# Kernel tuning notes

Hardware: AMD Instinct MI355X
Metric: run time of the kernel (lower is better)

The kernel has to match this reference:

```python
import jax, jax.numpy as jnp
import numpy as np

N = 50000          # site nodes
L = 32             # max URL token length
E = 64             # embed_size
H = 128            # hidden_size
E_SIM = 800000     # edges per relation in blocks
E_SUB = 200000     # 'sim' edges classified at the end
NEG = 0.01         # LeakyReLU negative slope

def leaky(x):
    return jnp.where(x >= 0, x, NEG * x)

def lstm_final(x, mask, Wih, Whh, b, reverse):
    # x: [N, L, E], mask: [N, L] bool. Returns packed-sequence final hidden [N, E].
    if reverse:
        x = x[:, ::-1, :]
        mask = mask[:, ::-1]
    h0 = jnp.zeros((x.shape[0], Whh.shape[1]), x.dtype)
    def step(carry, inp):
        h, c = carry
        xt, mt = inp
        g = xt @ Wih.T + h @ Whh.T + b
        i, f, gg, o = jnp.split(g, 4, axis=-1)  # PyTorch gate order i,f,g,o
        cn = jax.nn.sigmoid(f) * c + jax.nn.sigmoid(i) * jnp.tanh(gg)
        hn = jax.nn.sigmoid(o) * jnp.tanh(cn)
        m = mt[:, None]
        return (jnp.where(m, hn, h), jnp.where(m, cn, c)), None
    (h, _), _ = jax.lax.scan(step, (h0, h0), (x.transpose(1, 0, 2), mask.T))
    return h

def graph_conv(h, src, dst, W, b):
    # DGL GraphConv, norm='both': D_dst^{-1/2} A D_src^{-1/2} h W + b  (degrees clamped to >=1)
    n = h.shape[0]
    ones = jnp.ones(src.shape[0], h.dtype)
    out_deg = jnp.clip(jax.ops.segment_sum(ones, src, num_segments=n), 1.0)
    in_deg = jnp.clip(jax.ops.segment_sum(ones, dst, num_segments=n), 1.0)
    feat = h * jax.lax.rsqrt(out_deg)[:, None]
    if W.shape[0] > W.shape[1]:
        feat = feat @ W  # project before gather/scatter when in_dim > out_dim (as DGL does)
        rst = jax.ops.segment_sum(feat[src], dst, num_segments=n)
    else:
        rst = jax.ops.segment_sum(feat[src], dst, num_segments=n) @ W
    return rst * jax.lax.rsqrt(in_deg)[:, None] + b

def setup_inputs():
    key = jax.random.key(0)
    ks = iter(jax.random.split(key, 64))
    def nrm(shape, scale=0.05):
        return jax.random.normal(next(ks), shape, dtype=jnp.float32) * scale
    inp = {}
    inp["inputs_s"] = jax.random.randint(next(ks), (N, L), 0, 128)
    lengths = jax.random.randint(next(ks), (N,), 1, L + 1)
    inp["inputs_sm"] = (jnp.arange(L)[None, :] < lengths[:, None]).astype(jnp.int32)
    inp["inputs_c"] = jax.random.randint(next(ks), (N, 1), 0, 101)
    inp["inputs_co"] = jax.random.randint(next(ks), (N, 1), 0, 92)
    inp["inputs_sl"] = jax.random.randint(next(ks), (N, 1), 0, 6)
    for name, m in [("sim_src", E_SIM), ("sim_dst", E_SIM), ("user_src", E_SIM),
                    ("user_dst", E_SIM), ("esub_src", E_SUB), ("esub_dst", E_SUB)]:
        inp[name] = jax.random.randint(next(ks), (m,), 0, N)
    inp["emb_url"] = nrm((128, E)); inp["emb_cat"] = nrm((101, E))
    inp["emb_country"] = nrm((92, E)); inp["emb_sl"] = nrm((6, E))
    for d in ("f", "b"):
        inp["Wih_" + d] = nrm((4 * E, E)); inp["Whh_" + d] = nrm((4 * E, E))
        inp["b_" + d] = nrm((4 * E,))  # b_ih + b_hh folded into one bias
    inp["fc_W"] = nrm((E, 2 * E)); inp["fc_b"] = nrm((E,))
    for i, din in enumerate([4 * E, H]):
        for rel in ("sim", "user"):
            inp["gcn%d_%s_W" % (i, rel)] = nrm((din, H))
            inp["gcn%d_%s_b" % (i, rel)] = nrm((H,))
    inp["cls_W1"] = nrm((H, 2 * H)); inp["cls_b1"] = nrm((H,))
    inp["bn_g"] = jnp.ones((H,), jnp.float32); inp["bn_b"] = jnp.zeros((H,), jnp.float32)
    inp["cls_W2"] = nrm((2, H)); inp["cls_b2"] = nrm((2,))
    return inp

def reference(inputs_s, inputs_sm, inputs_c, inputs_co, inputs_sl,
              sim_src, sim_dst, user_src, user_dst, esub_src, esub_dst,
              emb_url, emb_cat, emb_country, emb_sl,
              Wih_f, Whh_f, b_f, Wih_b, Whh_b, b_b, fc_W, fc_b,
              gcn0_sim_W, gcn0_sim_b, gcn0_user_W, gcn0_user_b,
              gcn1_sim_W, gcn1_sim_b, gcn1_user_W, gcn1_user_b,
              cls_W1, cls_b1, bn_g, bn_b, cls_W2, cls_b2):
    mask = inputs_sm.astype(bool)
    x = emb_url[inputs_s]                                # [N, L, E]
    hf = lstm_final(x, mask, Wih_f, Whh_f, b_f, False)   # h_n[0]
    hb = lstm_final(x, mask, Wih_b, Whh_b, b_b, True)    # h_n[1]
    h_url = leaky(jnp.concatenate([hf, hb], -1) @ fc_W.T + fc_b)  # dropout = identity (eval)
    h = jnp.concatenate([h_url, emb_cat[inputs_c[:, 0]],
                         emb_country[inputs_co[:, 0]], emb_sl[inputs_sl[:, 0]]], -1)  # [N, 4E]
    layers = [(gcn0_sim_W, gcn0_sim_b, gcn0_user_W, gcn0_user_b),
              (gcn1_sim_W, gcn1_sim_b, gcn1_user_W, gcn1_user_b)]
    for Ws, bs, Wu, bu in layers:  # HeteroGraphConv aggregate='sum'
        h = leaky(graph_conv(h, sim_src, sim_dst, Ws, bs)
                  + graph_conv(h, user_src, user_dst, Wu, bu))
    feat = jnp.concatenate([h[esub_src], h[esub_dst]], -1)  # [E_SUB, 2H]
    z = feat @ cls_W1.T + cls_b1
    z = (z - z.mean(0)) * jax.lax.rsqrt(z.var(0) + 1e-5) * bn_g + bn_b  # BatchNorm1d (batch stats)
    z = jnp.maximum(z, 0.0)
    return z @ cls_W2.T + cls_b2
```

## Files before the change

### kernel.cpp

```cpp
#include <hip/hip_runtime.h>
#include <hip/hip_bf16.h>
#include <stdint.h>

#define N_NODES 50000
#define SEQ_L   32
#define NE_BIG  800000
#define NE_SUB  200000
#define DSTRIDE 64

typedef __hip_bfloat16 bf16;
typedef unsigned short u16;
typedef _Float16 f16;
typedef _Float16 v8h __attribute__((ext_vector_type(8)));
typedef float v4f __attribute__((ext_vector_type(4)));

__device__ __forceinline__ float b2f(bf16 x) { return __bfloat162float(x); }
__device__ __forceinline__ float leakyf(float v) { return v >= 0.f ? v : 0.01f * v; }
__device__ __forceinline__ u16 f2h_bits(float x) { f16 h = (f16)x; u16 b; __builtin_memcpy(&b, &h, 2); return b; }
__device__ __forceinline__ float h2f(u16 b) { f16 h; __builtin_memcpy(&h, &b, 2); return (float)h; }
__device__ __forceinline__ uint pack2h(float a, float b) { return (uint)f2h_bits(a) | ((uint)f2h_bits(b) << 16); }

__device__ __forceinline__ float ldf(const void* p, int i, int isbf) {
  return isbf ? b2f(((const bf16*)p)[i]) : ((const float*)p)[i];
}

__device__ __forceinline__ int detect_isbf(const u16* __restrict__ u) {
  __shared__ int insane;
  if (threadIdx.x == 0) insane = 0;
  __syncthreads();
  int expo = (u[threadIdx.x * 2] >> 7) & 0xFF;
  if (expo >= 147) atomicAdd(&insane, 1);
  __syncthreads();
  return insane == 0;
}

struct PrepArgs {
  const void* Whh_f; const void* Whh_b; const void* fc_W; const void* cls_W1;
  const void* g0sW; const void* g0uW; const void* g1sW; const void* g1uW;
  const void* emb_cat; const void* emb_country; const void* emb_sl;
  const void* fc_b; const void* cls_b1; const void* g0sb; const void* g0ub;
  const void* g1sb; const void* g1ub; const void* bn_g; const void* bn_b;
  const void* cls_W2; const void* cls_b2;
  const void* emb_url; const void* Wih_f; const void* b_f; const void* Wih_b; const void* b_b;
  f16* Whh_h; u16* Bfc; u16* BW1; u16* Bg0; u16* Bg1;
  u16* embc_h; u16* embco_h; u16* embs_h;
  float* fcb; float* b1; float* g0sbP; float* g0ubP; float* g1sbP; float* g1ubP;
  float* bngP; float* bnbP; float* W2P; float* b2P;
  int* dflag;
  float* Xperm;
  const int* sm; int* lens; int* cnt33;
  const int* s0; const int* d0; const int* s1; const int* d1;
  int* cnt4; int* col0; int* col1;
};

__global__ __launch_bounds__(256) void prep_graph_kernel(PrepArgs A) {
  const int b = blockIdx.x;
  const int t = threadIdx.x;
  const int NBL = (N_NODES + 255) / 256;
  const int NBE = (NE_BIG + 255) / 256;

  if (b >= 1186) {
    int rel = (b - 1186) / NBE;
    int e = ((b - 1186) % NBE) * 256 + t;
    if (e >= NE_BIG) return;
    const int* s = rel ? A.s1 : A.s0;
    const int* d = rel ? A.d1 : A.d0;
    int* col = rel ? A.col1 : A.col0;
    int* base = A.cnt4 + (size_t)rel * 2 * N_NODES;
    int sv = s[e], dv = d[e];
    atomicAdd(&base[sv], 1);
    int p = atomicAdd(&base[N_NODES + dv], 1);
    if (p < DSTRIDE) col[(size_t)dv * DSTRIDE + p] = sv;
    return;
  }
  if (b >= 990) {
    int i = (b - 990) * 256 + t;
    if (i >= N_NODES) return;
    int len = 0;
#pragma unroll
    for (int tt = 0; tt < SEQ_L; ++tt) len += A.sm[i * SEQ_L + tt];
    A.lens[i] = len;
    atomicAdd(&A.cnt33[len], 1);
    return;
  }

  const int isbf = detect_isbf((const u16*)A.emb_url);
  auto cpy = [&](const void* s, float* d, int n, int boff) {
    int i = (b - boff) * 256 + t;
    if (i < n) d[i] = ldf(s, i, isbf);
  };
  auto cvh = [&](const void* s, u16* d, int n, int boff) {
    int i = (b - boff) * 256 + t;
    if (i < n) d[i] = f2h_bits(ldf(s, i, isbf));
  };
  auto trh = [&](const void* s, u16* d, int R, int C, int KOFF, int boff) {
    int i = (b - boff) * 256 + t;
    if (i < R * C) { int r = i / C, c = i % C; d[c * 256 + KOFF + r] = f2h_bits(ldf(s, i, isbf)); }
  };
  if      (b <   64) cvh(A.Whh_f, (u16*)A.Whh_h, 16384, 0);
  else if (b <  128) cvh(A.Whh_b, (u16*)(A.Whh_h + 16384), 16384, 64);
  else if (b <  160) cvh(A.fc_W, A.Bfc, 8192, 128);
  else if (b <  288) cvh(A.cls_W1, A.BW1, 32768, 160);
  else if (b <  416) trh(A.g0sW, A.Bg0, 256, 128, 0, 288);
  else if (b <  544) trh(A.g0uW, A.Bg0 + 128 * 256, 256, 128, 0, 416);
  else if (b <  608) trh(A.g1sW, A.Bg1, 128, 128, 0, 544);
  else if (b <  672) trh(A.g1uW, A.Bg1, 128, 128, 128, 608);
  else if (b <  698) cvh(A.emb_cat, A.embc_h, 6464, 672);
  else if (b <  721) cvh(A.emb_country, A.embco_h, 5888, 698);
  else if (b <  723) cvh(A.emb_sl, A.embs_h, 384, 721);
  else if (b <  724) cpy(A.fc_b, A.fcb, 64, 723);
  else if (b <  725) cpy(A.cls_b1, A.b1, 128, 724);
  else if (b <  726) cpy(A.g0sb, A.g0sbP, 128, 725);
  else if (b <  727) cpy(A.g0ub, A.g0ubP, 128, 726);
  else if (b <  728) cpy(A.g1sb, A.g1sbP, 128, 727);
  else if (b <  729) cpy(A.g1ub, A.g1ubP, 128, 728);
  else if (b <  730) cpy(A.bn_g, A.bngP, 128, 729);
  else if (b <  731) cpy(A.bn_b, A.bnbP, 128, 730);
  else if (b <  732) cpy(A.cls_W2, A.W2P, 256, 731);
  else if (b <  733) { cpy(A.cls_b2, A.b2P, 2, 732); if (t == 0) A.dflag[0] = isbf; }
  else if (b <  989) {
    int bb = b - 733;
    int dir = bb >> 7;
    int v = bb & 127;
    const void* Wih = dir ? A.Wih_b : A.Wih_f;
    const void* bias = dir ? A.b_b : A.b_f;
    __shared__ float embL[64];
    if (t < 64) embL[t] = ldf(A.emb_url, v * 64 + t, isbf);
    __syncthreads();
    float acc = ldf(bias, t, isbf);
#pragma unroll 8
    for (int j = 0; j < 64; ++j) acc += embL[j] * ldf(Wih, t * 64 + j, isbf);
    int g = t >> 6, unit = t & 63;
    A.Xperm[(size_t)dir * 128 * 256 + v * 256 + unit * 4 + g] = acc;
  }
}
#define PG_BLOCKS (1186 + 2 * 3125)

__global__ __launch_bounds__(256) void permfill_rsq_kernel(
    const int* __restrict__ lens, const int* __restrict__ cnt33, int* __restrict__ cur33,
    int* __restrict__ perm,
    const int* __restrict__ cnt4, float* __restrict__ rsq4)
{
  const int b = blockIdx.x, t = threadIdx.x;
  const int NBL = (N_NODES + 255) / 256;
  if (b < NBL) {
    int i = b * 256 + t;
    if (i >= N_NODES) return;
    int len = lens[i];
    int base = 0;
    for (int l = len + 1; l <= SEQ_L; ++l) base += cnt33[l];
    int p = atomicAdd(&cur33[len], 1);
    perm[base + p] = i;
  } else {
    int i = (b - NBL) * 256 + t;
    if (i >= 4 * N_NODES) return;
    int c = cnt4[i]; if (c < 1) c = 1;
    rsq4[i] = __builtin_amdgcn_rsqf((float)c);
  }
}
#define PR_BLOCKS (196 + 782)

__global__ __launch_bounds__(256, 4) void lstm_mfma_kernel(
    const int* __restrict__ perm, const int* __restrict__ lens,
    const int* __restrict__ toksg,
    const float* __restrict__ Xperm,
    const f16* __restrict__ Whh_h,
    u16* __restrict__ hcat_h,
    int nnodes)
{
  __shared__ __align__(16) f16 H[2][64 * 72];
  __shared__ int toksL[2][64];
  __shared__ int permL[64];
  __shared__ int lensL[64];
  __shared__ int smax;
  const int tid = threadIdx.x;
  const int w = tid >> 6;
  const int lane = tid & 63;
  const int quad = lane >> 4;
  const int lid = lane & 15;
  const int dir = blockIdx.y;

  if (tid < 64) {
    int gid = blockIdx.x * 64 + tid;
    int node = -1, len = 0;
    if (gid < nnodes) { node = perm[gid]; len = lens[node]; }
    permL[tid] = node; lensL[tid] = len;
  }
  if (tid == 0) smax = 0;
  for (int i = tid; i < 64 * 72; i += 256) { H[0][i] = (f16)0.f; H[1][i] = (f16)0.f; }
  __syncthreads();
  if (tid < 64 && lensL[tid] > 0) atomicMax(&smax, lensL[tid]);
  __syncthreads();
  const int tmax = smax;

  const f16* Wd = Whh_h + (size_t)dir * 256 * 64;
  v8h Bf[4][2];
#pragma unroll
  for (int g = 0; g < 4; ++g)
#pragma unroll
    for (int kf = 0; kf < 2; ++kf)
      Bf[g][kf] = *(const v8h*)(Wd + (g * 64 + w * 16 + lid) * 64 + kf * 32 + quad * 8);

  int lenv[16];
#pragma unroll
  for (int mt = 0; mt < 4; ++mt)
#pragma unroll
    for (int r = 0; r < 4; ++r) lenv[mt * 4 + r] = lensL[mt * 16 + quad * 4 + r];

  float creg[16];
  f16 hreg[16];
#pragma unroll
  for (int i = 0; i < 16; ++i) { creg[i] = 0.f; hreg[i] = (f16)0.f; }

  const float* Xp = Xperm + (size_t)dir * 128 * 256;

  if (tid < 64) {
    int len = lensL[tid];
    int tok = 0;
    if (len > 0) tok = toksg[(size_t)permL[tid] * SEQ_L + (dir ? (len - 1) : 0)];
    toksL[0][tid] = tok;
  }
  __syncthreads();

  for (int step = 0; step < tmax; ++step) {
    const int rb = step & 1, wb = rb ^ 1;
#pragma unroll
    for (int mt = 0; mt < 4; ++mt) {
      float4 xr[4];
#pragma unroll
      for (int r = 0; r < 4; ++r) {
        int nd = mt * 16 + quad * 4 + r;
        xr[r] = *(const float4*)(Xp + (size_t)toksL[rb][nd] * 256 + (w * 16 + lid) * 4);
      }
      const f16* hb = &H[rb][0];
      int arow = (mt * 16 + lid) * 72 + quad * 8;
      v8h a0 = *(const v8h*)(hb + arow);
      v8h a1 = *(const v8h*)(hb + arow + 32);
      v4f acc[4];
#pragma unroll
      for (int g = 0; g < 4; ++g) {
        v4f a = {0.f, 0.f, 0.f, 0.f};
        a = __builtin_amdgcn_mfma_f32_16x16x32_f16(a0, Bf[g][0], a, 0, 0, 0);
        a = __builtin_amdgcn_mfma_f32_16x16x32_f16(a1, Bf[g][1], a, 0, 0, 0);
        acc[g] = a;
      }
#pragma unroll
      for (int r = 0; r < 4; ++r) {
        int idx = mt * 4 + r;
        int nd = mt * 16 + quad * 4 + r;
        bool act = step < lenv[idx];
        float gi = acc[0][r] + xr[r].x;
        float gf = acc[1][r] + xr[r].y;
        float gG = acc[2][r] + xr[r].z;
        float go = acc[3][r] + xr[r].w;
        float A = __expf(-gi);
        float B = __expf(-gf);
        float C = __expf(-go);
        float D = __expf(2.f * fminf(gG, 15.f));
        float sf = __builtin_amdgcn_rcpf(1.f + B);
        float sitg = (D - 1.f) * __builtin_amdgcn_rcpf((1.f + A) * (D + 1.f));
        float cn = sf * creg[idx] + sitg;
        float E = __expf(2.f * fminf(cn, 15.f));
        float hn = (E - 1.f) * __builtin_amdgcn_rcpf((1.f + C) * (E + 1.f));
        if (act) { creg[idx] = cn; hreg[idx] = (f16)hn; }
        H[wb][nd * 72 + w * 16 + lid] = hreg[idx];
      }
    }
    if (tid < 64 && step + 1 < tmax) {
      int len = lensL[tid];
      int tok = 0;
      if (step + 1 < len) {
        int t = dir ? (len - 2 - step) : (step + 1);
        tok = toksg[(size_t)permL[tid] * SEQ_L + t];
      }
      toksL[wb][tid] = tok;
    }
    __syncthreads();
  }
#pragma unroll
  for (int mt = 0; mt < 4; ++mt)
#pragma unroll
    for (int r = 0; r < 4; ++r) {
      int nd = mt * 16 + quad * 4 + r;
      int gnode = permL[nd];
      if (gnode >= 0) {
        u16 bits; f16 hv = hreg[mt * 4 + r]; __builtin_memcpy(&bits, &hv, 2);
        hcat_h[(size_t)gnode * 128 + dir * 64 + w * 16 + lid] = bits;
      }
    }
}

template<int K, int COLS, int AMODE, bool LEAKY, int OHS, bool EMB, bool BNS>
__global__ __launch_bounds__(256) void mfma_gemm(
    const u16* __restrict__ Ah,
    const int* __restrict__ esrc, const int* __restrict__ edst, const u16* __restrict__ Fh,
    const u16* __restrict__ B,
    const float* __restrict__ bias, const float* __restrict__ bias2,
    const float* __restrict__ rs0, const float* __restrict__ rs1,
    u16* __restrict__ outh0, u16* __restrict__ outh1,
    const int* __restrict__ ic, const int* __restrict__ ico, const int* __restrict__ isl,
    const u16* __restrict__ ech, const u16* __restrict__ ecoh, const u16* __restrict__ eslh,
    float* __restrict__ bnsums,
    int nrows)
{
  constexpr int AST = K + 8;
  constexpr int ABYTES = 64 * AST * 2;
  constexpr int EBYTES = 64 * 129 * 4;
  constexpr int SBYTES = (ABYTES > EBYTES) ? ABYTES : EBYTES;
  __shared__ __align__(16) char smem[SBYTES];
  u16* As = (u16*)smem;
  float* Es = (float*)smem;
  __shared__ int idxL[128];
  __shared__ float bnred[BNS ? 512 : 1];

  const int tid = threadIdx.x;
  const int w = tid >> 6;
  const int lane = tid & 63;
  const int quad = lane >> 4;
  const int lid = lane & 15;
  const int r0 = blockIdx.x * 64;

  if (AMODE == 2) {
    if (tid < 64) {
      int row = r0 + tid;
      idxL[tid] = (row < nrows) ? esrc[row] : -1;
      idxL[64 + tid] = (row < nrows) ? edst[row] : -1;
    }
    __syncthreads();
    for (int idx = tid; idx < 64 * (K / 8); idx += 256) {
      int rn = idx / (K / 8), seg = idx % (K / 8);
      int half = seg >> 4, k8 = seg & 15;
      int base = idxL[half * 64 + rn];
      uint4 v = {0u, 0u, 0u, 0u};
      if (base >= 0) v = *(const uint4*)(Fh + (size_t)base * 128 + k8 * 8);
      *(uint4*)(As + rn * AST + seg * 8) = v;
    }
  } else {
    for (int idx = tid; idx < 64 * (K / 8); idx += 256) {
      int rn = idx / (K / 8), c8 = idx % (K / 8);
      int row = r0 + rn;
      uint4 v = {0u, 0u, 0u, 0u};
      if (row < nrows) v = *(const uint4*)(Ah + (size_t)row * K + c8 * 8);
      *(uint4*)(As + rn * AST + c8 * 8) = v;
    }
  }
  __syncthreads();

  constexpr int NT = COLS / 16;
  v4f acc[NT];
#pragma unroll
  for (int i = 0; i < NT; ++i) acc[i] = (v4f){0.f, 0.f, 0.f, 0.f};

  for (int kb = 0; kb < K / 32; ++kb) {
    v8h a = *(const v8h*)((const f16*)As + (w * 16 + lid) * AST + kb * 32 + quad * 8);
#pragma unroll
    for (int ct = 0; ct < NT; ++ct) {
      v8h b = *(const v8h*)((const f16*)B + (size_t)(ct * 16 + lid) * K + kb * 32 + quad * 8);
      acc[ct] = __builtin_amdgcn_mfma_f32_16x16x32_f16(a, b, acc[ct], 0, 0, 0);
    }
  }

  constexpr int NH = (COLS > 128) ? 2 : 1;
  constexpr int CH = COLS / NH;
  float bs = 0.f, bs2 = 0.f;
#pragma unroll
  for (int h = 0; h < NH; ++h) {
    __syncthreads();
#pragma unroll
    for (int ct = 0; ct < CH / 16; ++ct) {
      int ctg = h * (CH / 16) + ct;
#pragma unroll
      for (int r = 0; r < 4; ++r)
        Es[(w * 16 + quad * 4 + r) * 129 + ct * 16 + lid] = acc[ctg][r];
    }
    __syncthreads();
    for (int idx = tid; idx < 64 * CH; idx += 256) {
      int rn = idx / CH, c = idx % CH;
      int row = r0 + rn;
      float v = 0.f;
      if (row < nrows) {
        v = Es[rn * 129 + c];
        if (bias) v += bias[h * CH + c];
        if (bias2) v += bias2[h * CH + c];
        if (LEAKY) v = leakyf(v);
        const float* rs = (h == 0) ? rs0 : rs1;
        if (rs) v *= rs[row];
        u16* oh = (h == 0) ? outh0 : outh1;
        oh[(size_t)row * OHS + c] = f2h_bits(v);
      }
      if (BNS) { bs += v; bs2 += v * v; }
    }
  }
  if (BNS) {
    bnred[tid] = bs;
    bnred[256 + tid] = bs2;
    __syncthreads();
    if (tid < 128) {
      atomicAdd(&bnsums[tid], bnred[tid] + bnred[tid + 128]);
      atomicAdd(&bnsums[128 + tid], bnred[256 + tid] + bnred[384 + tid]);
    }
  }
  if (EMB) {
    for (int idx = tid; idx < 64 * 192; idx += 256) {
      int rn = idx / 192, j = idx % 192;
      int row = r0 + rn;
      if (row >= nrows) continue;
      u16 v;
      if (j < 64)       v = ech [ic [row] * 64 + j];
      else if (j < 128) v = ecoh[ico[row] * 64 + (j - 64)];
      else              v = eslh[isl[row] * 64 + (j - 128)];
      outh0[(size_t)row * OHS + 64 + j] = v;
    }
  }
}

__global__ __launch_bounds__(256) void gather_merge0_kernel(
    const int* __restrict__ colS, const int* __restrict__ cntS, const u16* __restrict__ Ps,
    const int* __restrict__ colU, const int* __restrict__ cntU, const u16* __restrict__ Pu,
    const float* __restrict__ rsS, const float* __restrict__ rsU,
    const float* __restrict__ bS, const float* __restrict__ bU,
    u16* __restrict__ outh, int nnodes)
{
  int wave = threadIdx.x >> 6;
  int lane = threadIdx.x & 63;
  int node = __builtin_amdgcn_readfirstlane(blockIdx.x * 4 + wave);
  if (node >= nnodes) return;
  const uint* PS2 = (const uint*)Ps;
  const uint* PU2 = (const uint*)Pu;
  float2 aS = make_float2(0.f, 0.f), aU = make_float2(0.f, 0.f);
  {
    const int* col = colS + (size_t)node * DSTRIDE;
    int cnt = min(cntS[node], DSTRIDE);
    int e = 0;
    for (; e + 4 <= cnt; e += 4) {
      uint v0 = PS2[(size_t)col[e] * 64 + lane];
      uint v1 = PS2[(size_t)col[e + 1] * 64 + lane];
      uint v2 = PS2[(size_t)col[e + 2] * 64 + lane];
      uint v3 = PS2[(size_t)col[e + 3] * 64 + lane];
      aS.x += h2f((u16)v0) + h2f((u16)v1) + h2f((u16)v2) + h2f((u16)v3);
      aS.y += h2f((u16)(v0 >> 16)) + h2f((u16)(v1 >> 16)) + h2f((u16)(v2 >> 16)) + h2f((u16)(v3 >> 16));
    }
    for (; e < cnt; ++e) {
      uint v = PS2[(size_t)col[e] * 64 + lane];
      aS.x += h2f((u16)v); aS.y += h2f((u16)(v >> 16));
    }
  }
  {
    const int* col = colU + (size_t)node * DSTRIDE;
    int cnt = min(cntU[node], DSTRIDE);
    int e = 0;
    for (; e + 4 <= cnt; e += 4) {
      uint v0 = PU2[(size_t)col[e] * 64 + lane];
      uint v1 = PU2[(size_t)col[e + 1] * 64 + lane];
      uint v2 = PU2[(size_t)col[e + 2] * 64 + lane];
      uint v3 = PU2[(size_t)col[e + 3] * 64 + lane];
      aU.x += h2f((u16)v0) + h2f((u16)v1) + h2f((u16)v2) + h2f((u16)v3);
      aU.y += h2f((u16)(v0 >> 16)) + h2f((u16)(v1 >> 16)) + h2f((u16)(v2 >> 16)) + h2f((u16)(v3 >> 16));
    }
    for (; e < cnt; ++e) {
      uint v = PU2[(size_t)col[e] * 64 + lane];
      aU.x += h2f((u16)v); aU.y += h2f((u16)(v >> 16));
    }
  }
  float rS = rsS[node], rU = rsU[node];
  float2 bsv = ((const float2*)bS)[lane];
  float2 buv = ((const float2*)bU)[lane];
  float o0 = leakyf(aS.x * rS + bsv.x + aU.x * rU + buv.x);
  float o1 = leakyf(aS.y * rS + bsv.y + aU.y * rU + buv.y);
  ((uint*)outh)[(size_t)node * 64 + lane] = pack2h(o0, o1);
}

__global__ __launch_bounds__(256) void gather_cat1_kernel(
    const int* __restrict__ colS, const int* __restrict__ cntS,
    const int* __restrict__ colU, const int* __restrict__ cntU,
    const u16* __restrict__ Fh,
    const float* __restrict__ rsoutS, const float* __restrict__ rsoutU,
    const float* __restrict__ rsinS, const float* __restrict__ rsinU,
    u16* __restrict__ Acat, int nnodes)
{
  int wave = threadIdx.x >> 6;
  int lane = threadIdx.x & 63;
  int node = __builtin_amdgcn_readfirstlane(blockIdx.x * 4 + wave);
  if (node >= nnodes) return;
  const uint* F2 = (const uint*)Fh;
  float2 aS = make_float2(0.f, 0.f), aU = make_float2(0.f, 0.f);
  {
    const int* col = colS + (size_t)node * DSTRIDE;
    int cnt = min(cntS[node], DSTRIDE);
    int e = 0;
    for (; e + 2 <= cnt; e += 2) {
      int s0 = col[e], s1 = col[e + 1];
      float c0 = rsoutS[s0], c1 = rsoutS[s1];
      uint v0 = F2[(size_t)s0 * 64 + lane];
      uint v1 = F2[(size_t)s1 * 64 + lane];
      aS.x += c0 * h2f((u16)v0) + c1 * h2f((u16)v1);
      aS.y += c0 * h2f((u16)(v0 >> 16)) + c1 * h2f((u16)(v1 >> 16));
    }
    for (; e < cnt; ++e) {
      int s = col[e]; float c = rsoutS[s];
      uint v = F2[(size_t)s * 64 + lane];
      aS.x += c * h2f((u16)v); aS.y += c * h2f((u16)(v >> 16));
    }
  }
  {
    const int* col = colU + (size_t)node * DSTRIDE;
    int cnt = min(cntU[node], DSTRIDE);
    int e = 0;
    for (; e + 2 <= cnt; e += 2) {
      int s0 = col[e], s1 = col[e + 1];
      float c0 = rsoutU[s0], c1 = rsoutU[s1];
      uint v0 = F2[(size_t)s0 * 64 + lane];
      uint v1 = F2[(size_t)s1 * 64 + lane];
      aU.x += c0 * h2f((u16)v0) + c1 * h2f((u16)v1);
      aU.y += c0 * h2f((u16)(v0 >> 16)) + c1 * h2f((u16)(v1 >> 16));
    }
    for (; e < cnt; ++e) {
      int s = col[e]; float c = rsoutU[s];
      uint v = F2[(size_t)s * 64 + lane];
      aU.x += c * h2f((u16)v); aU.y += c * h2f((u16)(v >> 16));
    }
  }
  float rs = rsinS[node], ru = rsinU[node];
  ((uint*)Acat)[(size_t)node * 128 + lane] = pack2h(aS.x * rs, aS.y * rs);
  ((uint*)Acat)[(size_t)node * 128 + 64 + lane] = pack2h(aU.x * ru, aU.y * ru);
}

__global__ __launch_bounds__(256) void out_kernel(
    const u16* __restrict__ zh, const float* __restrict__ bnsums,
    const float* __restrict__ g, const float* __restrict__ bb, float M,
    const float* __restrict__ W2, const float* __restrict__ b2,
    void* __restrict__ out, int Mi, const int* __restrict__ flag)
{
  __shared__ float lds[128 * 65];
  __shared__ float red[64 * 8];
  __shared__ float ssL[256];
  const int tid = threadIdx.x;
  const int n = tid & 63;
  const int q = __builtin_amdgcn_readfirstlane(tid >> 6);
  const int r0 = blockIdx.x * 64;
  if (tid < 128) {
    float mean = bnsums[tid] / M;
    float var = bnsums[128 + tid] / M - mean * mean;
    float sc = g[tid] * __builtin_amdgcn_rsqf(var + 1e-5f);
    ssL[tid] = sc;
    ssL[128 + tid] = bb[tid] - mean * sc;
  }
  for (int idx = tid; idx < 64 * 128; idx += 256) {
    int rn = idx >> 7, j = idx & 127;
    int row = r0 + rn;
    lds[j * 65 + rn] = (row < Mi) ? h2f(zh[(size_t)row * 128 + j]) : 0.f;
  }
  __syncthreads();
  float a0 = 0.f, a1 = 0.f;
#pragma unroll 8
  for (int jj = 0; jj < 32; ++jj) {
    int j = q * 32 + jj;
    float y = lds[j * 65 + n] * ssL[j] + ssL[128 + j];
    y = y > 0.f ? y : 0.f;
    a0 += y * W2[j];
    a1 += y * W2[128 + j];
  }
  red[n * 8 + q * 2 + 0] = a0;
  red[n * 8 + q * 2 + 1] = a1;
  __syncthreads();
  if (q == 0 && (r0 + n) < Mi) {
    float o0 = red[n * 8] + red[n * 8 + 2] + red[n * 8 + 4] + red[n * 8 + 6] + b2[0];
    float o1 = red[n * 8 + 1] + red[n * 8 + 3] + red[n * 8 + 5] + red[n * 8 + 7] + b2[1];
    size_t oi = (size_t)(r0 + n) * 2;
    if (*flag) {
      ((bf16*)out)[oi + 0] = __float2bfloat16(o0);
      ((bf16*)out)[oi + 1] = __float2bfloat16(o1);
    } else {
      ((float*)out)[oi + 0] = o0;
      ((float*)out)[oi + 1] = o1;
    }
  }
}

extern "C" void kernel_launch(void* const* d_in, const int* in_sizes, int n_in,
                              void* d_out, int out_size, void* d_ws, size_t ws_size,
                              hipStream_t stream) {
  (void)in_sizes; (void)n_in; (void)out_size; (void)ws_size;
  const int N = N_NODES;
  const int* inputs_s  = (const int*)d_in[0];
  const int* inputs_sm = (const int*)d_in[1];
  const int* inputs_c  = (const int*)d_in[2];
  const int* inputs_co = (const int*)d_in[3];
  const int* inputs_sl = (const int*)d_in[4];
  const int* sim_src   = (const int*)d_in[5];
  const int* sim_dst   = (const int*)d_in[6];
  const int* user_src  = (const int*)d_in[7];
  const int* user_dst  = (const int*)d_in[8];
  const int* esub_src  = (const int*)d_in[9];
  const int* esub_dst  = (const int*)d_in[10];

  char* base = (char*)d_ws;
  size_t off = 0;
  auto alloc = [&](size_t bytes) -> char* {
    char* p = base + off;
    off += (bytes + 255) & ~(size_t)255;
    return p;
  };
  int* dflag    = (int*)alloc(256);
  f16* Whh_h    = (f16*)alloc(2 * 256 * 64 * 2);
  float* Xperm  = (float*)alloc(2 * 128 * 256 * 4);
  u16* Bfc      = (u16*)alloc(64 * 128 * 2);
  u16* BW1      = (u16*)alloc(128 * 256 * 2);
  u16* Bg0      = (u16*)alloc(256 * 256 * 2);
  u16* Bg1      = (u16*)alloc(128 * 256 * 2);
  u16* P_embc_h = (u16*)alloc(6464 * 2);
  u16* P_embco_h= (u16*)alloc(5888 * 2);
  u16* P_embs_h = (u16*)alloc(384 * 2);
  float* P_fcb  = (float*)alloc(64 * 4);
  float* P_b1   = (float*)alloc(128 * 4);
  float* P_g0sb = (float*)alloc(128 * 4);
  float* P_g0ub = (float*)alloc(128 * 4);
  float* P_g1sb = (float*)alloc(128 * 4);
  float* P_g1ub = (float*)alloc(128 * 4);
  float* P_bng  = (float*)alloc(128 * 4);
  float* P_bnb  = (float*)alloc(128 * 4);
  float* P_W2   = (float*)alloc(256 * 4);
  float* P_b2   = (float*)alloc(2 * 4);
  int* lens     = (int*)alloc((size_t)N * 4);
  int* perm     = (int*)alloc((size_t)N * 4);
  float* rsq4   = (float*)alloc((size_t)4 * N * 4);
  char* zbase   = alloc((size_t)4 * N * 4 + 3 * 256 + 1024);
  int* cnt4     = (int*)zbase;
  int* cnt33    = (int*)(zbase + (size_t)4 * N * 4);
  int* cur33    = cnt33 + 64;
  float* bnsums = (float*)(zbase + (size_t)4 * N * 4 + 512);
  const size_t zbytes = (size_t)4 * N * 4 + 3 * 256 + 1024;
  char* bufA = alloc((size_t)N * 256 * 4);
  char* bufB = alloc((size_t)N * 256 * 2);
  char* bufC = alloc((size_t)N * 256 * 2);
  char* bufE = alloc((size_t)N * 128 * 2);
  u16* h_h     = (u16*)bufA;
  u16* zh      = (u16*)bufA;
  int* col_sim = (int*)(bufA + (size_t)N * 256 * 2);
  int* col_usr = (int*)(bufA + (size_t)N * 256 * 2 + (size_t)N * DSTRIDE * 4);
  u16* hcat_h = (u16*)bufB;
  u16* h1_h   = (u16*)bufB;
  u16* Ps_h   = (u16*)bufC;
  u16* Pu_h   = Ps_h + (size_t)N * 128;
  u16* Acat   = (u16*)bufC;
  u16* F_h    = (u16*)bufE;

  const int NB64 = (N + 63) / 64;
  const int NBZ  = (NE_SUB + 63) / 64;

  hipMemsetAsync(zbase, 0, zbytes, stream);

  PrepArgs PA;
  PA.Whh_f = d_in[16]; PA.Whh_b = d_in[19]; PA.fc_W = d_in[21]; PA.cls_W1 = d_in[31];
  PA.g0sW = d_in[23]; PA.g0uW = d_in[25]; PA.g1sW = d_in[27]; PA.g1uW = d_in[29];
  PA.emb_cat = d_in[12]; PA.emb_country = d_in[13]; PA.emb_sl = d_in[14];
  PA.fc_b = d_in[22]; PA.cls_b1 = d_in[32]; PA.g0sb = d_in[24]; PA.g0ub = d_in[26];
  PA.g1sb = d_in[28]; PA.g1ub = d_in[30]; PA.bn_g = d_in[33]; PA.bn_b = d_in[34];
  PA.cls_W2 = d_in[35]; PA.cls_b2 = d_in[36];
  PA.emb_url = d_in[11]; PA.Wih_f = d_in[15]; PA.b_f = d_in[17]; PA.Wih_b = d_in[18]; PA.b_b = d_in[20];
  PA.Whh_h = Whh_h; PA.Bfc = Bfc; PA.BW1 = BW1; PA.Bg0 = Bg0; PA.Bg1 = Bg1;
  PA.embc_h = P_embc_h; PA.embco_h = P_embco_h; PA.embs_h = P_embs_h;
  PA.fcb = P_fcb; PA.b1 = P_b1; PA.g0sbP = P_g0sb; PA.g0ubP = P_g0ub; PA.g1sbP = P_g1sb; PA.g1ubP = P_g1ub;
  PA.bngP = P_bng; PA.bnbP = P_bnb; PA.W2P = P_W2; PA.b2P = P_b2;
  PA.dflag = dflag; PA.Xperm = Xperm;
  PA.sm = inputs_sm; PA.lens = lens; PA.cnt33 = cnt33;
  PA.s0 = sim_src; PA.d0 = sim_dst; PA.s1 = user_src; PA.d1 = user_dst;
  PA.cnt4 = cnt4; PA.col0 = col_sim; PA.col1 = col_usr;
  prep_graph_kernel<<<PG_BLOCKS, 256, 0, stream>>>(PA);

  permfill_rsq_kernel<<<PR_BLOCKS, 256, 0, stream>>>(lens, cnt33, cur33, perm, cnt4, rsq4);

  lstm_mfma_kernel<<<dim3(NB64, 2), 256, 0, stream>>>(perm, lens, inputs_s, Xperm, Whh_h, hcat_h, N);

  mfma_gemm<128, 64, 1, true, 256, true, false><<<NB64, 256, 0, stream>>>(
      hcat_h, nullptr, nullptr, nullptr, Bfc, P_fcb, nullptr, nullptr, nullptr,
      h_h, nullptr, inputs_c, inputs_co, inputs_sl, P_embc_h, P_embco_h, P_embs_h, nullptr, N);

  mfma_gemm<256, 256, 1, false, 128, false, false><<<NB64, 256, 0, stream>>>(
      h_h, nullptr, nullptr, nullptr, Bg0, nullptr, nullptr, rsq4, rsq4 + 2 * N,
      Ps_h, Pu_h, nullptr, nullptr, nullptr, nullptr, nullptr, nullptr, nullptr, N);

  gather_merge0_kernel<<<(N + 3) / 4, 256, 0, stream>>>(col_sim, cnt4 + N, Ps_h,
                                                        col_usr, cnt4 + 3 * N, Pu_h,
                                                        rsq4 + N, rsq4 + 3 * N, P_g0sb, P_g0ub, h1_h, N);

  gather_cat1_kernel<<<(N + 3) / 4, 256, 0, stream>>>(col_sim, cnt4 + N, col_usr, cnt4 + 3 * N, h1_h,
                                                      rsq4, rsq4 + 2 * N, rsq4 + N, rsq4 + 3 * N, Acat, N);

  mfma_gemm<256, 128, 1, true, 128, false, false><<<NB64, 256, 0, stream>>>(
      Acat, nullptr, nullptr, nullptr, Bg1, P_g1sb, P_g1ub, nullptr, nullptr,
      F_h, nullptr, nullptr, nullptr, nullptr, nullptr, nullptr, nullptr, nullptr, N);

  mfma_gemm<256, 128, 2, false, 128, false, true><<<NBZ, 256, 0, stream>>>(
      nullptr, esub_src, esub_dst, F_h, BW1, P_b1, nullptr, nullptr, nullptr,
      zh, nullptr, nullptr, nullptr, nullptr, nullptr, nullptr, nullptr, bnsums, NE_SUB);

  out_kernel<<<NBZ, 256, 0, stream>>>(zh, bnsums, P_bng, P_bnb, (float)NE_SUB,
                                      P_W2, P_b2, d_out, NE_SUB, dflag);
}
```

Before: 1.130 ms.

## Overlap graph CSR build with LSTM tail via work-stealing; compute rsqrt on the fly

Moves the edge-counting and column-list build out of the prep kernel. Each LSTM block, once its recurrence finishes, takes edge chunks from a global atomic counter, so graph construction fills idle CUs while the length-sorted LSTM blocks finish unevenly. It also drops the separate rsqrt-degree pass and buffer, computing rsqrt from the raw counts inside the GEMM and gather kernels. The cost is extra rsqrt work per gathered neighbor, and the scatter atomics now compete with LSTM blocks that are still running.

```diff
diff --git a/kernel.cpp b/kernel.cpp
--- a/kernel.cpp
+++ b/kernel.cpp
@@ -7,6 +7,7 @@
 #define NE_BIG  800000
 #define NE_SUB  200000
 #define DSTRIDE 64
+#define NCHUNK  6250
 
 typedef __hip_bfloat16 bf16;
 typedef unsigned short u16;
@@ -19,6 +20,7 @@
 __device__ __forceinline__ u16 f2h_bits(float x) { f16 h = (f16)x; u16 b; __builtin_memcpy(&b, &h, 2); return b; }
 __device__ __forceinline__ float h2f(u16 b) { f16 h; __builtin_memcpy(&h, &b, 2); return (float)h; }
 __device__ __forceinline__ uint pack2h(float a, float b) { return (uint)f2h_bits(a) | ((uint)f2h_bits(b) << 16); }
+__device__ __forceinline__ float rsqcnt(int c) { return __builtin_amdgcn_rsqf((float)(c < 1 ? 1 : c)); }
 
 __device__ __forceinline__ float ldf(const void* p, int i, int isbf) {
   return isbf ? b2f(((const bf16*)p)[i]) : ((const float*)p)[i];
@@ -49,32 +51,14 @@
   int* dflag;
   float* Xperm;
   const int* sm; int* lens; int* cnt33;
-  const int* s0; const int* d0; const int* s1; const int* d1;
-  int* cnt4; int* col0; int* col1;
 };
 
-__global__ __launch_bounds__(256) void prep_graph_kernel(PrepArgs A) {
+__global__ __launch_bounds__(256) void prep_kernel(PrepArgs A) {
   const int b = blockIdx.x;
   const int t = threadIdx.x;
-  const int NBL = (N_NODES + 255) / 256;
-  const int NBE = (NE_BIG + 255) / 256;
-
-  if (b >= 1186) {
-    int rel = (b - 1186) / NBE;
-    int e = ((b - 1186) % NBE) * 256 + t;
-    if (e >= NE_BIG) return;
-    const int* s = rel ? A.s1 : A.s0;
-    const int* d = rel ? A.d1 : A.d0;
-    int* col = rel ? A.col1 : A.col0;
-    int* base = A.cnt4 + (size_t)rel * 2 * N_NODES;
-    int sv = s[e], dv = d[e];
-    atomicAdd(&base[sv], 1);
-    int p = atomicAdd(&base[N_NODES + dv], 1);
-    if (p < DSTRIDE) col[(size_t)dv * DSTRIDE + p] = sv;
-    return;
-  }
-  if (b >= 990) {
-    int i = (b - 990) * 256 + t;
+
+  if (b >= 989) {
+    int i = (b - 989) * 256 + t;
     if (i >= N_NODES) return;
     int len = 0;
 #pragma unroll
@@ -118,7 +102,7 @@
   else if (b <  731) cpy(A.bn_b, A.bnbP, 128, 730);
   else if (b <  732) cpy(A.cls_W2, A.W2P, 256, 731);
   else if (b <  733) { cpy(A.cls_b2, A.b2P, 2, 732); if (t == 0) A.dflag[0] = isbf; }
-  else if (b <  989) {
+  else {
     int bb = b - 733;
     int dir = bb >> 7;
     int v = bb & 127;
@@ -134,45 +118,39 @@
     A.Xperm[(size_t)dir * 128 * 256 + v * 256 + unit * 4 + g] = acc;
   }
 }
-#define PG_BLOCKS (1186 + 2 * 3125)
-
-__global__ __launch_bounds__(256) void permfill_rsq_kernel(
+#define PREP_BLOCKS 1185
+
+__global__ __launch_bounds__(256) void permfill_kernel(
     const int* __restrict__ lens, const int* __restrict__ cnt33, int* __restrict__ cur33,
-    int* __restrict__ perm,
-    const int* __restrict__ cnt4, float* __restrict__ rsq4)
+    int* __restrict__ perm)
 {
-  const int b = blockIdx.x, t = threadIdx.x;
-  const int NBL = (N_NODES + 255) / 256;
-  if (b < NBL) {
-    int i = b * 256 + t;
-    if (i >= N_NODES) return;
-    int len = lens[i];
-    int base = 0;
-    for (int l = len + 1; l <= SEQ_L; ++l) base += cnt33[l];
-    int p = atomicAdd(&cur33[len], 1);
-    perm[base + p] = i;
-  } else {
-    int i = (b - NBL) * 256 + t;
-    if (i >= 4 * N_NODES) return;
-    int c = cnt4[i]; if (c < 1) c = 1;
-    rsq4[i] = __builtin_amdgcn_rsqf((float)c);
-  }
-}
-#define PR_BLOCKS (196 + 782)
-
-__global__ __launch_bounds__(256, 4) void lstm_mfma_kernel(
+  int i = blockIdx.x * 256 + threadIdx.x;
+  if (i >= N_NODES) return;
+  int len = lens[i];
+  int base = 0;
+  for (int l = len + 1; l <= SEQ_L; ++l) base += cnt33[l];
+  int p = atomicAdd(&cur33[len], 1);
+  perm[base + p] = i;
+}
+
+__global__ __launch_bounds__(256, 4) void lstm_graph_kernel(
     const int* __restrict__ perm, const int* __restrict__ lens,
     const int* __restrict__ toksg,
     const float* __restrict__ Xperm,
     const f16* __restrict__ Whh_h,
     u16* __restrict__ hcat_h,
-    int nnodes)
+    int nnodes,
+    const int* __restrict__ s0, const int* __restrict__ d0,
+    const int* __restrict__ s1, const int* __restrict__ d1,
+    int* __restrict__ cnt4, int* __restrict__ col0, int* __restrict__ col1,
+    int* __restrict__ workctr)
 {
   __shared__ __align__(16) f16 H[2][64 * 72];
   __shared__ int toksL[2][64];
   __shared__ int permL[64];
   __shared__ int lensL[64];
   __shared__ int smax;
+  __shared__ int chunkL;
   const int tid = threadIdx.x;
   const int w = tid >> 6;
   const int lane = tid & 63;
@@ -288,9 +266,29 @@
         hcat_h[(size_t)gnode * 128 + dir * 64 + w * 16 + lid] = bits;
       }
     }
-}
-
-template<int K, int COLS, int AMODE, bool LEAKY, int OHS, bool EMB, bool BNS>
+
+  for (;;) {
+    __syncthreads();
+    if (tid == 0) chunkL = atomicAdd(workctr, 1);
+    __syncthreads();
+    int c = chunkL;
+    if (c >= NCHUNK) break;
+    int rel = c / 3125;
+    int e = (c % 3125) * 256 + tid;
+    if (e < NE_BIG) {
+      const int* s = rel ? s1 : s0;
+      const int* d = rel ? d1 : d0;
+      int* col = rel ? col1 : col0;
+      int* base = cnt4 + (size_t)rel * 2 * N_NODES;
+      int sv = s[e], dv = d[e];
+      atomicAdd(&base[sv], 1);
+      int p = atomicAdd(&base[N_NODES + dv], 1);
+      if (p < DSTRIDE) col[(size_t)dv * DSTRIDE + p] = sv;
+    }
+  }
+}
+
+template<int K, int COLS, int AMODE, bool LEAKY, int OHS, bool EMB, bool BNS, bool RSQ>
 __global__ __launch_bounds__(256) void mfma_gemm(
     const u16* __restrict__ Ah,
     const int* __restrict__ esrc, const int* __restrict__ edst, const u16* __restrict__ Fh,
@@ -384,7 +382,10 @@
         if (bias2) v += bias2[h * CH + c];
         if (LEAKY) v = leakyf(v);
         const float* rs = (h == 0) ? rs0 : rs1;
-        if (rs) v *= rs[row];
+        if (rs) {
+          if (RSQ) v *= rsqcnt(((const int*)rs)[row]);
+          else v *= rs[row];
+        }
         u16* oh = (h == 0) ? outh0 : outh1;
         oh[(size_t)row * OHS + c] = f2h_bits(v);
       }
@@ -417,7 +418,6 @@
 __global__ __launch_bounds__(256) void gather_merge0_kernel(
     const int* __restrict__ colS, const int* __restrict__ cntS, const u16* __restrict__ Ps,
     const int* __restrict__ colU, const int* __restrict__ cntU, const u16* __restrict__ Pu,
-    const float* __restrict__ rsS, const float* __restrict__ rsU,
     const float* __restrict__ bS, const float* __restrict__ bU,
     u16* __restrict__ outh, int nnodes)
 {
@@ -428,9 +428,10 @@
   const uint* PS2 = (const uint*)Ps;
   const uint* PU2 = (const uint*)Pu;
   float2 aS = make_float2(0.f, 0.f), aU = make_float2(0.f, 0.f);
+  int cS = cntS[node], cU = cntU[node];
   {
     const int* col = colS + (size_t)node * DSTRIDE;
-    int cnt = min(cntS[node], DSTRIDE);
+    int cnt = min(cS, DSTRIDE);
     int e = 0;
     for (; e + 4 <= cnt; e += 4) {
       uint v0 = PS2[(size_t)col[e] * 64 + lane];
@@ -447,7 +448,7 @@
   }
   {
     const int* col = colU + (size_t)node * DSTRIDE;
-    int cnt = min(cntU[node], DSTRIDE);
+    int cnt = min(cU, DSTRIDE);
     int e = 0;
     for (; e + 4 <= cnt; e += 4) {
       uint v0 = PU2[(size_t)col[e] * 64 + lane];
@@ -462,7 +463,7 @@
       aU.x += h2f((u16)v); aU.y += h2f((u16)(v >> 16));
     }
   }
-  float rS = rsS[node], rU = rsU[node];
+  float rS = rsqcnt(cS), rU = rsqcnt(cU);
   float2 bsv = ((const float2*)bS)[lane];
   float2 buv = ((const float2*)bU)[lane];
   float o0 = leakyf(aS.x * rS + bsv.x + aU.x * rU + buv.x);
@@ -474,8 +475,7 @@
     const int* __restrict__ colS, const int* __restrict__ cntS,
     const int* __restrict__ colU, const int* __restrict__ cntU,
     const u16* __restrict__ Fh,
-    const float* __restrict__ rsoutS, const float* __restrict__ rsoutU,
-    const float* __restrict__ rsinS, const float* __restrict__ rsinU,
+    const int* __restrict__ cntOutS, const int* __restrict__ cntOutU,
     u16* __restrict__ Acat, int nnodes)
 {
   int wave = threadIdx.x >> 6;
@@ -484,43 +484,44 @@
   if (node >= nnodes) return;
   const uint* F2 = (const uint*)Fh;
   float2 aS = make_float2(0.f, 0.f), aU = make_float2(0.f, 0.f);
+  int cS = cntS[node], cU = cntU[node];
   {
     const int* col = colS + (size_t)node * DSTRIDE;
-    int cnt = min(cntS[node], DSTRIDE);
+    int cnt = min(cS, DSTRIDE);
     int e = 0;
     for (; e + 2 <= cnt; e += 2) {
       int s0 = col[e], s1 = col[e + 1];
-      float c0 = rsoutS[s0], c1 = rsoutS[s1];
+      float c0 = rsqcnt(cntOutS[s0]), c1 = rsqcnt(cntOutS[s1]);
       uint v0 = F2[(size_t)s0 * 64 + lane];
       uint v1 = F2[(size_t)s1 * 64 + lane];
       aS.x += c0 * h2f((u16)v0) + c1 * h2f((u16)v1);
       aS.y += c0 * h2f((u16)(v0 >> 16)) + c1 * h2f((u16)(v1 >> 16));
     }
     for (; e < cnt; ++e) {
-      int s = col[e]; float c = rsoutS[s];
+      int s = col[e]; float c = rsqcnt(cntOutS[s]);
       uint v = F2[(size_t)s * 64 + lane];
       aS.x += c * h2f((u16)v); aS.y += c * h2f((u16)(v >> 16));
     }
   }
   {
     const int* col = colU + (size_t)node * DSTRIDE;
-    int cnt = min(cntU[node], DSTRIDE);
+    int cnt = min(cU, DSTRIDE);
     int e = 0;
     for (; e + 2 <= cnt; e += 2) {
       int s0 = col[e], s1 = col[e + 1];
-      float c0 = rsoutU[s0], c1 = rsoutU[s1];
+      float c0 = rsqcnt(cntOutU[s0]), c1 = rsqcnt(cntOutU[s1]);
       uint v0 = F2[(size_t)s0 * 64 + lane];
       uint v1 = F2[(size_t)s1 * 64 + lane];
       aU.x += c0 * h2f((u16)v0) + c1 * h2f((u16)v1);
       aU.y += c0 * h2f((u16)(v0 >> 16)) + c1 * h2f((u16)(v1 >> 16));
     }
     for (; e < cnt; ++e) {
-      int s = col[e]; float c = rsoutU[s];
+      int s = col[e]; float c = rsqcnt(cntOutU[s]);
       uint v = F2[(size_t)s * 64 + lane];
       aU.x += c * h2f((u16)v); aU.y += c * h2f((u16)(v >> 16));
     }
   }
-  float rs = rsinS[node], ru = rsinU[node];
+  float rs = rsqcnt(cS), ru = rsqcnt(cU);
   ((uint*)Acat)[(size_t)node * 128 + lane] = pack2h(aS.x * rs, aS.y * rs);
   ((uint*)Acat)[(size_t)node * 128 + 64 + lane] = pack2h(aU.x * ru, aU.y * ru);
 }
@@ -623,12 +624,12 @@
   float* P_b2   = (float*)alloc(2 * 4);
   int* lens     = (int*)alloc((size_t)N * 4);
   int* perm     = (int*)alloc((size_t)N * 4);
-  float* rsq4   = (float*)alloc((size_t)4 * N * 4);
   char* zbase   = alloc((size_t)4 * N * 4 + 3 * 256 + 1024);
   int* cnt4     = (int*)zbase;
   int* cnt33    = (int*)(zbase + (size_t)4 * N * 4);
   int* cur33    = cnt33 + 64;
   float* bnsums = (float*)(zbase + (size_t)4 * N * 4 + 512);
+  int* workctr  = (int*)(zbase + (size_t)4 * N * 4 + 512 + 256);
   const size_t zbytes = (size_t)4 * N * 4 + 3 * 256 + 1024;
   char* bufA = alloc((size_t)N * 256 * 4);
   char* bufB = alloc((size_t)N * 256 * 2);
@@ -664,34 +665,35 @@
   PA.bngP = P_bng; PA.bnbP = P_bnb; PA.W2P = P_W2; PA.b2P = P_b2;
   PA.dflag = dflag; PA.Xperm = Xperm;
   PA.sm = inputs_sm; PA.lens = lens; PA.cnt33 = cnt33;
-  PA.s0 = sim_src; PA.d0 = sim_dst; PA.s1 = user_src; PA.d1 = user_dst;
-  PA.cnt4 = cnt4; PA.col0 = col_sim; PA.col1 = col_usr;
-  prep_graph_kernel<<<PG_BLOCKS, 256, 0, stream>>>(PA);
-
-  permfill_rsq_kernel<<<PR_BLOCKS, 256, 0, stream>>>(lens, cnt33, cur33, perm, cnt4, rsq4);
-
-  lstm_mfma_kernel<<<dim3(NB64, 2), 256, 0, stream>>>(perm, lens, inputs_s, Xperm, Whh_h, hcat_h, N);
-
-  mfma_gemm<128, 64, 1, true, 256, true, false><<<NB64, 256, 0, stream>>>(
+  prep_kernel<<<PREP_BLOCKS, 256, 0, stream>>>(PA);
+
+  permfill_kernel<<<(N + 255) / 256, 256, 0, stream>>>(lens, cnt33, cur33, perm);
+
+  lstm_graph_kernel<<<dim3(NB64, 2), 256, 0, stream>>>(perm, lens, inputs_s, Xperm, Whh_h, hcat_h, N,
+                                                       sim_src, sim_dst, user_src, user_dst,
+                                                       cnt4, col_sim, col_usr, workctr);
+
+  mfma_gemm<128, 64, 1, true, 256, true, false, false><<<NB64, 256, 0, stream>>>(
       hcat_h, nullptr, nullptr, nullptr, Bfc, P_fcb, nullptr, nullptr, nullptr,
       h_h, nullptr, inputs_c, inputs_co, inputs_sl, P_embc_h, P_embco_h, P_embs_h, nullptr, N);
 
-  mfma_gemm<256, 256, 1, false, 128, false, false><<<NB64, 256, 0, stream>>>(
-      h_h, nullptr, nullptr, nullptr, Bg0, nullptr, nullptr, rsq4, rsq4 + 2 * N,
+  mfma_gemm<256, 256, 1, false, 128, false, false, true><<<NB64, 256, 0, stream>>>(
+      h_h, nullptr, nullptr, nullptr, Bg0, nullptr, nullptr,
+      (const float*)cnt4, (const float*)(cnt4 + 2 * N),
       Ps_h, Pu_h, nullptr, nullptr, nullptr, nullptr, nullptr, nullptr, nullptr, N);
 
   gather_merge0_kernel<<<(N + 3) / 4, 256, 0, stream>>>(col_sim, cnt4 + N, Ps_h,
                                                         col_usr, cnt4 + 3 * N, Pu_h,
-                                                        rsq4 + N, rsq4 + 3 * N, P_g0sb, P_g0ub, h1_h, N);
+                                                        P_g0sb, P_g0ub, h1_h, N);
 
   gather_cat1_kernel<<<(N + 3) / 4, 256, 0, stream>>>(col_sim, cnt4 + N, col_usr, cnt4 + 3 * N, h1_h,
-                                                      rsq4, rsq4 + 2 * N, rsq4 + N, rsq4 + 3 * N, Acat, N);
-
-  mfma_gemm<256, 128, 1, true, 128, false, false><<<NB64, 256, 0, stream>>>(
+                                                      cnt4, cnt4 + 2 * N, Acat, N);
+
+  mfma_gemm<256, 128, 1, true, 128, false, false, false><<<NB64, 256, 0, stream>>>(
       Acat, nullptr, nullptr, nullptr, Bg1, P_g1sb, P_g1ub, nullptr, nullptr,
       F_h, nullptr, nullptr, nullptr, nullptr, nullptr, nullptr, nullptr, nullptr, N);
 
-  mfma_gemm<256, 128, 2, false, 128, false, true><<<NBZ, 256, 0, stream>>>(
+  mfma_gemm<256, 128, 2, false, 128, false, true, false><<<NBZ, 256, 0, stream>>>(
       nullptr, esub_src, esub_dst, F_h, BW1, P_b1, nullptr, nullptr, nullptr,
       zh, nullptr, nullptr, nullptr, nullptr, nullptr, nullptr, nullptr, bnsums, NE_SUB);
 
```

Result: no change. 1.149 ms (+1.7%).
